# Performance work log

Measured on AMD Instinct MI355X. Metric: run time of the kernel, lower is better.

Reference implementation:

```python
import jax, jax.numpy as jnp
import numpy as np

N = 100000       # num nodes
E = 1600000      # num edges (avg degree 16)
IN_DIM = 256
EMB_DIM = 128
K = 2            # nlayers: number of propagation steps


def setup_inputs() -> dict:
    key = jax.random.key(0)
    k1, k2, k3, k4, k5 = jax.random.split(key, 5)
    x = jax.random.normal(k1, (N, IN_DIM), dtype=jnp.float32)
    # glorot-initialized linear weight + zero bias
    scale = jnp.sqrt(6.0 / (IN_DIM + EMB_DIM))
    W = jax.random.uniform(k2, (IN_DIM, EMB_DIM), minval=-scale, maxval=scale, dtype=jnp.float32)
    b = jnp.zeros((EMB_DIM,), dtype=jnp.float32)
    edge_src = jax.random.randint(k3, (E,), 0, N, dtype=jnp.int32)
    edge_dst = jax.random.randint(k4, (E,), 0, N, dtype=jnp.int32)
    # normalized-adjacency-like edge weights (positive, ~1/deg scale)
    edge_w = jax.random.uniform(k5, (E,), dtype=jnp.float32) * (1.0 / 16.0)
    return {"x": x, "W": W, "b": b, "edge_src": edge_src, "edge_dst": edge_dst, "edge_w": edge_w}


def reference(x, W, b, edge_src, edge_dst, edge_w):
    # dropout is identity in eval mode; linear + relu
    h = jax.nn.relu(x @ W + b)  # [N, EMB_DIM]
    # k-step sparse propagation: h <- g @ h, g given as COO edge list
    for _ in range(K):
        msg = h[edge_src] * edge_w[:, None]                     # [E, EMB_DIM]
        h = jax.ops.segment_sum(msg, edge_dst, num_segments=N)  # [N, EMB_DIM]
    return h
```

## Files before the change

### kernel.cpp

```cpp
#include <hip/hip_runtime.h>

#define IN_DIM 256
#define EMB 128
#define BKT_SHIFT 9
#define BKT_NODES 512
#define BINE 4096
#define SCAP 12288

typedef __attribute__((ext_vector_type(8))) short short8;
typedef __attribute__((ext_vector_type(4))) float f32x4;

__device__ __forceinline__ unsigned short bf16rtne(float f) {
    unsigned int u = __float_as_uint(f);
    return (unsigned short)((u + 0x7fffu + ((u >> 16) & 1u)) >> 16);
}

__device__ __forceinline__ unsigned int packbf2(float lo, float hi) {
    return ((unsigned int)bf16rtne(hi) << 16) | (unsigned int)bf16rtne(lo);
}

__device__ __forceinline__ short8 pack8(float4 f0, float4 f1) {
    union { uint4 u; short8 s; } U;
    asm("v_cvt_pk_bf16_f32 %0, %1, %2" : "=v"(U.u.x) : "v"(f0.x), "v"(f0.y));
    asm("v_cvt_pk_bf16_f32 %0, %1, %2" : "=v"(U.u.y) : "v"(f0.z), "v"(f0.w));
    asm("v_cvt_pk_bf16_f32 %0, %1, %2" : "=v"(U.u.z) : "v"(f1.x), "v"(f1.y));
    asm("v_cvt_pk_bf16_f32 %0, %1, %2" : "=v"(U.u.w) : "v"(f1.z), "v"(f1.w));
    return U.s;
}


__global__ __launch_bounds__(256) void prep(const float* __restrict__ W,
                                            unsigned short* __restrict__ wtg,
                                            const float* __restrict__ x,
                                            unsigned short* __restrict__ xb, int total8,
                                            const int* __restrict__ dst,
                                            int* __restrict__ ghist, int E) {
    int t = threadIdx.x;
    int gsz = gridDim.x * 256;
    int gid = blockIdx.x * 256 + t;
    for (int i = gid; i < IN_DIM * EMB; i += gsz) {
        int c = i & 127;
        int k = i >> 7;
        wtg[c * 256 + k] = bf16rtne(W[(size_t)k * 128 + c]);
    }
    for (int i = gid; i < total8; i += gsz) {
        const float4* s = (const float4*)(x + (size_t)i * 8);
        *(short8*)(xb + (size_t)i * 8) = pack8(s[0], s[1]);
    }
    __shared__ int h[256];
    h[t] = 0;
    __syncthreads();
    for (int i = gid; i < E; i += gsz) atomicAdd(&h[dst[i] >> BKT_SHIFT], 1);
    __syncthreads();
    if (h[t]) atomicAdd(&ghist[t], h[t]);
}

__global__ __launch_bounds__(256) void bucket_scan(const int* __restrict__ ghist,
                                                   int* __restrict__ bucket_off,
                                                   int* __restrict__ gcursor,
                                                   int* __restrict__ row_ptr,
                                                   int NB, int N, int E) {
    __shared__ int s[256];
    int t = threadIdx.x;
    int v = (t < NB) ? ghist[t] : 0;
    s[t] = v;
    __syncthreads();
    for (int off = 1; off < 256; off <<= 1) {
        int u = (t >= off) ? s[t - off] : 0;
        __syncthreads();
        s[t] += u;
        __syncthreads();
    }
    int excl = s[t] - v;
    if (t < NB) {
        bucket_off[t] = excl;
        gcursor[t] = excl;
    }
    if (t == 0) {
        bucket_off[NB] = E;
        row_ptr[N] = E;
    }
}


__global__ __launch_bounds__(512) void bin_scatter(const int* __restrict__ src,
                                                   const int* __restrict__ dst,
                                                   const float* __restrict__ w,
                                                   int* __restrict__ gcursor,
                                                   int2* __restrict__ binned, int E) {
    __shared__ int h[256];
    __shared__ int lbase[256];
    __shared__ int gbase[256];
    __shared__ int lcur[256];
    __shared__ int2 stage[BINE];
    __shared__ unsigned char sb[BINE];
    int t = threadIdx.x;
    int e0 = blockIdx.x * BINE;
    int e1 = min(E, e0 + BINE);
    int n = e1 - e0;

    int ed[8], es[8];
    float ewv[8];
#pragma unroll
    for (int j = 0; j < 8; ++j) {
        int i = e0 + t + j * 512;
        if (i < e1) {
            ed[j] = dst[i];
            es[j] = src[i];
            ewv[j] = w[i];
        } else
            ed[j] = -1;
    }
    if (t < 256) h[t] = 0;
    __syncthreads();
#pragma unroll
    for (int j = 0; j < 8; ++j)
        if (ed[j] >= 0) atomicAdd(&h[ed[j] >> BKT_SHIFT], 1);
    __syncthreads();
    int v = 0;
    if (t < 256) {
        v = h[t];
        lbase[t] = v;
    }
    __syncthreads();
    for (int off = 1; off < 256; off <<= 1) {
        int u = 0;
        if (t < 256 && t >= off) u = lbase[t - off];
        __syncthreads();
        if (t < 256) lbase[t] += u;
        __syncthreads();
    }
    if (t < 256) {
        lbase[t] -= v;
        lcur[t] = lbase[t];
        gbase[t] = v ? atomicAdd(&gcursor[t], v) : 0;
    }
    __syncthreads();
#pragma unroll
    for (int j = 0; j < 8; ++j) {
        if (ed[j] >= 0) {
            int b = ed[j] >> BKT_SHIFT;
            int p = atomicAdd(&lcur[b], 1);
            int2 r;
            r.x = es[j] | ((ed[j] & (BKT_NODES - 1)) << 17);
            r.y = __float_as_int(ewv[j]);
            stage[p] = r;
            sb[p] = (unsigned char)b;
        }
    }
    __syncthreads();
    for (int i = t; i < n; i += 512) {
        int b = sb[i];
        binned[gbase[b] + (i - lbase[b])] = stage[i];
    }
}


__global__ __launch_bounds__(1024) void bucket_sort(const int2* __restrict__ binned,
                                                    const int* __restrict__ bucket_off,
                                                    int2* __restrict__ sorted,
                                                    int* __restrict__ row_ptr, int N) {
    __shared__ int cnt[BKT_NODES];
    __shared__ int cur[BKT_NODES];
    __shared__ int scn[BKT_NODES];
    __shared__ int2 stage[SCAP];
    int t = threadIdx.x;
    int b = blockIdx.x;
    int node0 = b << BKT_SHIFT;
    int nn = min(BKT_NODES, N - node0);
    int beg = bucket_off[b];
    int endb = bucket_off[b + 1];
    int n = endb - beg;
    if (t < BKT_NODES) cnt[t] = 0;
    __syncthreads();
    for (int i = beg + t; i < endb; i += 1024) {
        int ld = ((unsigned int)binned[i].x) >> 17;
        atomicAdd(&cnt[ld], 1);
    }
    __syncthreads();
    int v = 0;
    if (t < BKT_NODES) {
        v = cnt[t];
        scn[t] = v;
    }
    __syncthreads();
    for (int off = 1; off < BKT_NODES; off <<= 1) {
        int u = 0;
        if (t < BKT_NODES && t >= off) u = scn[t - off];
        __syncthreads();
        if (t < BKT_NODES) scn[t] += u;
        __syncthreads();
    }
    if (t < BKT_NODES) {
        int excl = scn[t] - v;
        cur[t] = excl;
        if (t < nn) row_ptr[node0 + t] = beg + excl;
    }
    __syncthreads();
    if (n <= SCAP) {
        for (int i = beg + t; i < endb; i += 1024) {
            int2 r = binned[i];
            int ld = ((unsigned int)r.x) >> 17;
            int p = atomicAdd(&cur[ld], 1);
            r.x &= 0x1FFFF;
            stage[p] = r;
        }
        __syncthreads();
        for (int i = t; i < n; i += 1024) sorted[beg + i] = stage[i];
    } else {
        for (int i = beg + t; i < endb; i += 1024) {
            int2 r = binned[i];
            int ld = ((unsigned int)r.x) >> 17;
            int p = atomicAdd(&cur[ld], 1);
            r.x &= 0x1FFFF;
            sorted[beg + p] = r;
        }
    }
}


__global__ __launch_bounds__(256) void gemm_mfma(const unsigned short* __restrict__ xb,
                                                 const unsigned short* __restrict__ wtg,
                                                 const float* __restrict__ bias,
                                                 unsigned short* __restrict__ hbf, int N) {
    __shared__ unsigned short As[128][64];
    __shared__ unsigned short Bs[128][64];
    int tid = threadIdx.x;
    int wv = tid >> 6;
    int lane = tid & 63;
    int lr = lane & 15;
    int lg = lane >> 4;
    int wr = wv * 32;
    int row0 = blockIdx.x * 128;

    f32x4 acc[2][8];
#pragma unroll
    for (int m = 0; m < 2; ++m)
#pragma unroll
        for (int n = 0; n < 8; ++n) acc[m][n] = (f32x4){0.f, 0.f, 0.f, 0.f};

    int p0 = wv * 4 * 64 + lane;

    for (int kb = 0; kb < IN_DIM; kb += 64) {
#pragma unroll
        for (int i = 0; i < 4; ++i) {
            int p = p0 + i * 64;
            int r = p >> 3;
            int c = p & 7;
            int cs = (c ^ (r & 7)) * 8;
            int gr = row0 + r;
            if (gr >= N) gr = N - 1;
            const unsigned short* ga = xb + (size_t)gr * IN_DIM + kb + cs;
            __builtin_amdgcn_global_load_lds(
                (const __attribute__((address_space(1))) void*)ga,
                (__attribute__((address_space(3))) void*)((char*)&As[0][0] + (size_t)(wv * 4 + i) * 1024),
                16, 0, 0);
            const unsigned short* gb = wtg + (size_t)r * IN_DIM + kb + cs;
            __builtin_amdgcn_global_load_lds(
                (const __attribute__((address_space(1))) void*)gb,
                (__attribute__((address_space(3))) void*)((char*)&Bs[0][0] + (size_t)(wv * 4 + i) * 1024),
                16, 0, 0);
        }
        __syncthreads();

        short8 a[2][2];
#pragma unroll
        for (int m = 0; m < 2; ++m)
#pragma unroll
            for (int kk = 0; kk < 2; ++kk) {
                int r = wr + m * 16 + lr;
                int ch = kk * 4 + lg;
                a[m][kk] = *(const short8*)&As[r][((ch ^ (r & 7)) * 8)];
            }
#pragma unroll
        for (int n = 0; n < 8; ++n) {
            int cc = n * 16 + lr;
            int sw = cc & 7;
            short8 b0 = *(const short8*)&Bs[cc][(((0 * 4 + lg) ^ sw) * 8)];
            short8 b1 = *(const short8*)&Bs[cc][(((1 * 4 + lg) ^ sw) * 8)];
            acc[0][n] = __builtin_amdgcn_mfma_f32_16x16x32_bf16(a[0][0], b0, acc[0][n], 0, 0, 0);
            acc[0][n] = __builtin_amdgcn_mfma_f32_16x16x32_bf16(a[0][1], b1, acc[0][n], 0, 0, 0);
            acc[1][n] = __builtin_amdgcn_mfma_f32_16x16x32_bf16(a[1][0], b0, acc[1][n], 0, 0, 0);
            acc[1][n] = __builtin_amdgcn_mfma_f32_16x16x32_bf16(a[1][1], b1, acc[1][n], 0, 0, 0);
        }
        __syncthreads();
    }

#pragma unroll
    for (int n = 0; n < 8; ++n) {
        int c = n * 16 + lr;
        float bv = bias[c];
#pragma unroll
        for (int m = 0; m < 2; ++m) {
#pragma unroll
            for (int j = 0; j < 4; ++j) {
                int r = row0 + wr + m * 16 + lg * 4 + j;
                if (r < N) {
                    float v = fmaxf(acc[m][n][j] + bv, 0.f);
                    hbf[(size_t)r * EMB + c] = bf16rtne(v);
                }
            }
        }
    }
}


template <int OUTBF>
__global__ __launch_bounds__(256) void prop_g(const unsigned int* __restrict__ hin,
                                              void* __restrict__ hout,
                                              const int* __restrict__ rp,
                                              const int2* __restrict__ rec, int N) {
    int wvid = threadIdx.x >> 6;
    int lane = threadIdx.x & 63;
    int node = blockIdx.x * 4 + wvid;
    if (node >= N) return;
    int beg = __builtin_amdgcn_readfirstlane(rp[node]);
    int end = __builtin_amdgcn_readfirstlane(rp[node + 1]);
    float ax = 0.f, ay = 0.f;
    for (int c0 = beg; c0 < end; c0 += 64) {
        int cnt = end - c0;
        if (cnt > 64) cnt = 64;
        int li = lane < cnt ? lane : 0;
        int2 r = rec[c0 + li];
        for (int jb = 0; jb < cnt; jb += 16) {
            int ssrc[16];
            float sw[16];
#pragma unroll
            for (int k = 0; k < 16; ++k) {
                int jj = jb + k;
                int jc = jj < cnt ? jj : 0;
                ssrc[k] = __builtin_amdgcn_readlane(r.x, jc);
                float wv = __uint_as_float((unsigned int)__builtin_amdgcn_readlane(r.y, jc));
                sw[k] = (jj < cnt) ? wv : 0.f;
            }
            unsigned int g[16];
#pragma unroll
            for (int k = 0; k < 16; ++k) g[k] = hin[(size_t)ssrc[k] * 64 + lane];
#pragma unroll
            for (int k = 0; k < 16; ++k) {
                ax = fmaf(sw[k], __uint_as_float(g[k] << 16), ax);
                ay = fmaf(sw[k], __uint_as_float(g[k] & 0xffff0000u), ay);
            }
        }
    }
    if (OUTBF) {
        ((unsigned int*)hout)[(size_t)node * 64 + lane] = packbf2(ax, ay);
    } else {
        float2 o;
        o.x = ax;
        o.y = ay;
        ((float2*)hout)[(size_t)node * 64 + lane] = o;
    }
}


extern "C" void kernel_launch(void* const* d_in, const int* in_sizes, int n_in,
                              void* d_out, int out_size, void* d_ws, size_t ws_size,
                              hipStream_t stream) {
    const float* x = (const float*)d_in[0];
    const float* W = (const float*)d_in[1];
    const float* b = (const float*)d_in[2];
    const int* esrc = (const int*)d_in[3];
    const int* edst = (const int*)d_in[4];
    const float* ew = (const float*)d_in[5];
    int N = in_sizes[0] / IN_DIM;
    int E = in_sizes[3];
    int NB = (N + BKT_NODES - 1) >> BKT_SHIFT;

    char* p = (char*)d_ws;
    auto alloc = [&](size_t bytes) -> void* {
        void* r = (void*)p;
        p += (bytes + 255) & ~(size_t)255;
        return r;
    };
    unsigned short* hbf = (unsigned short*)alloc((size_t)N * EMB * 2);
    unsigned short* h1bf = (unsigned short*)alloc((size_t)N * EMB * 2);
    unsigned short* wtg = (unsigned short*)alloc((size_t)IN_DIM * EMB * 2);
    unsigned short* xbf = (unsigned short*)alloc((size_t)N * IN_DIM * 2);
    int* ghist = (int*)alloc(256 * 4);
    int* gcursor = (int*)alloc(256 * 4);
    int* bucket_off = (int*)alloc((size_t)(NB + 1) * 4);
    int* row_ptr = (int*)alloc((size_t)(N + 1) * 4);
    int2* binned = (int2*)alloc((size_t)E * 8);
    int2* sorted = (int2*)alloc((size_t)E * 8);

    hipMemsetAsync(ghist, 0, 256 * 4, stream);
    prep<<<2048, 256, 0, stream>>>(W, wtg, x, xbf, N * IN_DIM / 8, edst, ghist, E);
    bucket_scan<<<1, 256, 0, stream>>>(ghist, bucket_off, gcursor, row_ptr, NB, N, E);
    bin_scatter<<<(E + BINE - 1) / BINE, 512, 0, stream>>>(esrc, edst, ew, gcursor, binned, E);
    bucket_sort<<<NB, 1024, 0, stream>>>(binned, bucket_off, sorted, row_ptr, N);

    gemm_mfma<<<(N + 127) / 128, 256, 0, stream>>>(xbf, wtg, b, hbf, N);
    prop_g<1><<<(N + 3) / 4, 256, 0, stream>>>((const unsigned int*)hbf, h1bf, row_ptr, sorted, N);
    prop_g<0><<<(N + 3) / 4, 256, 0, stream>>>((const unsigned int*)h1bf, d_out, row_ptr, sorted, N);
}
```

Before: 244.1 us.

## Fuse fp32-to-bf16 conversion of x into GEMM tile loads

The separate pass that converted x to bf16 in the prep kernel is removed. The GEMM now loads fp32 x tiles straight into LDS with swizzled direct global-to-LDS loads and packs them to bf16 when building MFMA operands. This drops a full write and re-read of a bf16 copy of x, at the cost of twice the LDS footprint and load traffic per GEMM tile. The destination histogram loop is also vectorized to int4 reads, and the prep grid is halved.

```diff
diff --git a/kernel.cpp b/kernel.cpp
--- a/kernel.cpp
+++ b/kernel.cpp
@@ -31,8 +31,6 @@
 
 __global__ __launch_bounds__(256) void prep(const float* __restrict__ W,
                                             unsigned short* __restrict__ wtg,
-                                            const float* __restrict__ x,
-                                            unsigned short* __restrict__ xb, int total8,
                                             const int* __restrict__ dst,
                                             int* __restrict__ ghist, int E) {
     int t = threadIdx.x;
@@ -43,14 +41,18 @@
         int k = i >> 7;
         wtg[c * 256 + k] = bf16rtne(W[(size_t)k * 128 + c]);
     }
-    for (int i = gid; i < total8; i += gsz) {
-        const float4* s = (const float4*)(x + (size_t)i * 8);
-        *(short8*)(xb + (size_t)i * 8) = pack8(s[0], s[1]);
-    }
     __shared__ int h[256];
     h[t] = 0;
     __syncthreads();
-    for (int i = gid; i < E; i += gsz) atomicAdd(&h[dst[i] >> BKT_SHIFT], 1);
+    int nE4 = E >> 2;
+    for (int i = gid; i < nE4; i += gsz) {
+        int4 d = ((const int4*)dst)[i];
+        atomicAdd(&h[d.x >> BKT_SHIFT], 1);
+        atomicAdd(&h[d.y >> BKT_SHIFT], 1);
+        atomicAdd(&h[d.z >> BKT_SHIFT], 1);
+        atomicAdd(&h[d.w >> BKT_SHIFT], 1);
+    }
+    for (int i = (nE4 << 2) + gid; i < E; i += gsz) atomicAdd(&h[dst[i] >> BKT_SHIFT], 1);
     __syncthreads();
     if (h[t]) atomicAdd(&ghist[t], h[t]);
 }
@@ -219,11 +221,11 @@
 }
 
 
-__global__ __launch_bounds__(256) void gemm_mfma(const unsigned short* __restrict__ xb,
+__global__ __launch_bounds__(256) void gemm_mfma(const float* __restrict__ x,
                                                  const unsigned short* __restrict__ wtg,
                                                  const float* __restrict__ bias,
                                                  unsigned short* __restrict__ hbf, int N) {
-    __shared__ unsigned short As[128][64];
+    __shared__ float Asf[128][64];
     __shared__ unsigned short Bs[128][64];
     int tid = threadIdx.x;
     int wv = tid >> 6;
@@ -239,26 +241,29 @@
 #pragma unroll
         for (int n = 0; n < 8; ++n) acc[m][n] = (f32x4){0.f, 0.f, 0.f, 0.f};
 
-    int p0 = wv * 4 * 64 + lane;
-
     for (int kb = 0; kb < IN_DIM; kb += 64) {
 #pragma unroll
+        for (int i = 0; i < 8; ++i) {
+            int p = 256 * i + wv * 64 + lane;
+            int r = p >> 4;
+            int c = p & 15;
+            int gr = row0 + r;
+            if (gr >= N) gr = N - 1;
+            const float* ga = x + (size_t)gr * IN_DIM + kb + ((c ^ (r & 7)) << 2);
+            __builtin_amdgcn_global_load_lds(
+                (const __attribute__((address_space(1))) void*)ga,
+                (__attribute__((address_space(3))) void*)((char*)&Asf[0][0] + (size_t)(256 * i + wv * 64) * 16),
+                16, 0, 0);
+        }
+#pragma unroll
         for (int i = 0; i < 4; ++i) {
-            int p = p0 + i * 64;
+            int p = 256 * i + wv * 64 + lane;
             int r = p >> 3;
             int c = p & 7;
-            int cs = (c ^ (r & 7)) * 8;
-            int gr = row0 + r;
-            if (gr >= N) gr = N - 1;
-            const unsigned short* ga = xb + (size_t)gr * IN_DIM + kb + cs;
-            __builtin_amdgcn_global_load_lds(
-                (const __attribute__((address_space(1))) void*)ga,
-                (__attribute__((address_space(3))) void*)((char*)&As[0][0] + (size_t)(wv * 4 + i) * 1024),
-                16, 0, 0);
-            const unsigned short* gb = wtg + (size_t)r * IN_DIM + kb + cs;
+            const unsigned short* gb = wtg + (size_t)r * IN_DIM + kb + ((c ^ (r & 7)) * 8);
             __builtin_amdgcn_global_load_lds(
                 (const __attribute__((address_space(1))) void*)gb,
-                (__attribute__((address_space(3))) void*)((char*)&Bs[0][0] + (size_t)(wv * 4 + i) * 1024),
+                (__attribute__((address_space(3))) void*)((char*)&Bs[0][0] + (size_t)(256 * i + wv * 64) * 16),
                 16, 0, 0);
         }
         __syncthreads();
@@ -269,8 +274,11 @@
 #pragma unroll
             for (int kk = 0; kk < 2; ++kk) {
                 int r = wr + m * 16 + lr;
-                int ch = kk * 4 + lg;
-                a[m][kk] = *(const short8*)&As[r][((ch ^ (r & 7)) * 8)];
+                int s = r & 7;
+                int ch0 = kk * 8 + lg * 2;
+                float4 f0 = *(const float4*)&Asf[r][(ch0 ^ s) << 2];
+                float4 f1 = *(const float4*)&Asf[r][((ch0 + 1) ^ s) << 2];
+                a[m][kk] = pack8(f0, f1);
             }
 #pragma unroll
         for (int n = 0; n < 8; ++n) {
@@ -376,7 +384,6 @@
     unsigned short* hbf = (unsigned short*)alloc((size_t)N * EMB * 2);
     unsigned short* h1bf = (unsigned short*)alloc((size_t)N * EMB * 2);
     unsigned short* wtg = (unsigned short*)alloc((size_t)IN_DIM * EMB * 2);
-    unsigned short* xbf = (unsigned short*)alloc((size_t)N * IN_DIM * 2);
     int* ghist = (int*)alloc(256 * 4);
     int* gcursor = (int*)alloc(256 * 4);
     int* bucket_off = (int*)alloc((size_t)(NB + 1) * 4);
@@ -385,12 +392,12 @@
     int2* sorted = (int2*)alloc((size_t)E * 8);
 
     hipMemsetAsync(ghist, 0, 256 * 4, stream);
-    prep<<<2048, 256, 0, stream>>>(W, wtg, x, xbf, N * IN_DIM / 8, edst, ghist, E);
+    prep<<<1024, 256, 0, stream>>>(W, wtg, edst, ghist, E);
     bucket_scan<<<1, 256, 0, stream>>>(ghist, bucket_off, gcursor, row_ptr, NB, N, E);
     bin_scatter<<<(E + BINE - 1) / BINE, 512, 0, stream>>>(esrc, edst, ew, gcursor, binned, E);
     bucket_sort<<<NB, 1024, 0, stream>>>(binned, bucket_off, sorted, row_ptr, N);
 
-    gemm_mfma<<<(N + 127) / 128, 256, 0, stream>>>(xbf, wtg, b, hbf, N);
+    gemm_mfma<<<(N + 127) / 128, 256, 0, stream>>>(x, wtg, b, hbf, N);
     prop_g<1><<<(N + 3) / 4, 256, 0, stream>>>((const unsigned int*)hbf, h1bf, row_ptr, sorted, N);
     prop_g<0><<<(N + 3) / 4, 256, 0, stream>>>((const unsigned int*)h1bf, d_out, row_ptr, sorted, N);
 }
```

Result: faster. 219.7 us (-10.0%).
